# Performance work log

Measured on AMD Instinct MI355X. Metric: run time of the kernel, lower is better.

## Reference

```python
import jax, jax.numpy as jnp
import numpy as np

E, D, DFF = 8, 1024, 4096

def setup_inputs() -> dict:
    key = jax.random.key(0)
    ks = jax.random.split(key, 10)
    s = 0.02
    return {
        "x":  jax.random.normal(ks[0], (4, 2048, D), dtype=jnp.float32),
        "Wr": jax.random.normal(ks[1], (D, E), dtype=jnp.float32) * s,
        "br": jnp.zeros((E,), dtype=jnp.float32),
        "W1": jax.random.normal(ks[2], (E, D, DFF), dtype=jnp.float32) * s,
        "b1": jnp.zeros((E, DFF), dtype=jnp.float32),
        "W2": jax.random.normal(ks[3], (E, D, DFF), dtype=jnp.float32) * s,
        "b2": jnp.zeros((E, DFF), dtype=jnp.float32),
        "W3": jax.random.normal(ks[4], (E, DFF, D), dtype=jnp.float32) * s,
        "b3": jnp.zeros((E, D), dtype=jnp.float32),
    }

def reference(x, Wr, br, W1, b1, W2, b2, W3, b3):
    b, s, d = x.shape
    xt = x.reshape(b * s, d)                       # [T, D]
    logits = xt @ Wr + br                          # [T, E]
    pr, idx = jax.lax.top_k(logits, 2)             # [T, 2]
    w = jax.nn.softmax(pr, axis=-1)                # softmax over the 2 selected experts
    # combine weight per (token, expert): sum of routing weights where expert selected
    onehot = jax.nn.one_hot(idx, W1.shape[0], dtype=x.dtype)  # [T, 2, E]
    cw = jnp.einsum('tk,tke->te', w, onehot)       # [T, E]
    y = jnp.zeros_like(xt)
    for e in range(W1.shape[0]):                   # small fixed expert loop
        h = jax.nn.silu(xt @ W1[e] + b1[e]) * (xt @ W2[e] + b2[e])  # SwiGLU [T, DFF]
        y = y + (h @ W3[e] + b3[e]) * cw[:, e:e + 1]
    return y.reshape(b, s, d)
```

## Files before the change

### kernel.cpp

```cpp
#include <hip/hip_runtime.h>

#define T_TOK 8192
#define DIM   1024
#define DFF_  4096
#define NE    8
#define MAXT  144

typedef float  f32x4 __attribute__((ext_vector_type(4)));
typedef __bf16 b16x8 __attribute__((ext_vector_type(8)));

__device__ __forceinline__ unsigned short f2bf(float f) {
  union { float f; unsigned int u; } v; v.f = f;
  unsigned int r = v.u + 0x7fffu + ((v.u >> 16) & 1u);
  return (unsigned short)(r >> 16);
}

__device__ __forceinline__ void gload_lds16(const void* g, void* l) {
  __builtin_amdgcn_global_load_lds((const __attribute__((address_space(1))) void*)g,
                                   (__attribute__((address_space(3))) void*)l,
                                   16, 0, 0);
}

#define DRAIN_VMCNT() asm volatile("s_waitcnt vmcnt(0)" ::: "memory")

__global__ __launch_bounds__(256) void transpose_cvt(const float* __restrict__ src,
                                                     unsigned short* __restrict__ dst,
                                                     int R, int C) {
  __shared__ float tile[64][65];
  size_t mat = (size_t)blockIdx.z * R * C;
  int c0 = blockIdx.x * 64, r0 = blockIdx.y * 64;
  int lc = threadIdx.x & 63, q = threadIdx.x >> 6;
  const float* s = src + mat + (size_t)r0 * C + c0;
#pragma unroll
  for (int i = 0; i < 16; i++) {
    int r = q + i * 4;
    tile[r][lc] = s[(size_t)r * C + lc];
  }
  __syncthreads();
  unsigned short* d = dst + mat + (size_t)c0 * R + r0;
#pragma unroll
  for (int i = 0; i < 16; i++) {
    int cc = q + i * 4;
    d[(size_t)cc * R + lc] = f2bf(tile[lc][cc]);
  }
}

__global__ __launch_bounds__(256) void router_k(const float* __restrict__ x,
                                                const float* __restrict__ Wr,
                                                const float* __restrict__ br,
                                                unsigned short* __restrict__ Xbf,
                                                int* __restrict__ top2e,
                                                float* __restrict__ top2w) {
  int wid = threadIdx.x >> 6, lane = threadIdx.x & 63;
  int t = blockIdx.x * 4 + wid;
  const float* xr = x + (size_t)t * DIM;
  unsigned short* xb = Xbf + (size_t)t * DIM;
  float s[NE];
#pragma unroll
  for (int e = 0; e < NE; e++) s[e] = 0.f;
  for (int i = 0; i < DIM / 64; i++) {
    int dd = i * 64 + lane;
    float xv = xr[dd];
    xb[dd] = f2bf(xv);
    const float* w = Wr + (size_t)dd * NE;
#pragma unroll
    for (int e = 0; e < NE; e++) s[e] += xv * w[e];
  }
#pragma unroll
  for (int m = 32; m >= 1; m >>= 1) {
#pragma unroll
    for (int e = 0; e < NE; e++) s[e] += __shfl_xor(s[e], m, 64);
  }
  if (lane == 0) {
#pragma unroll
    for (int e = 0; e < NE; e++) s[e] += br[e];
    int e0 = 0;
#pragma unroll
    for (int e = 1; e < NE; e++) if (s[e] > s[e0]) e0 = e;
    int e1 = (e0 == 0) ? 1 : 0;
#pragma unroll
    for (int e = 0; e < NE; e++) if (e != e0 && s[e] > s[e1]) e1 = e;
    float w0 = 1.f / (1.f + expf(s[e1] - s[e0]));
    top2e[2 * t] = e0; top2e[2 * t + 1] = e1;
    top2w[2 * t] = w0; top2w[2 * t + 1] = 1.f - w0;
  }
}

__global__ __launch_bounds__(256) void count_k(const int* __restrict__ top2e,
                                               int* __restrict__ counts) {
  __shared__ int lcnt[NE];
  if (threadIdx.x < NE) lcnt[threadIdx.x] = 0;
  __syncthreads();
  int t = blockIdx.x * 256 + threadIdx.x;
  atomicAdd(&lcnt[top2e[2 * t]], 1);
  atomicAdd(&lcnt[top2e[2 * t + 1]], 1);
  __syncthreads();
  if (threadIdx.x < NE) atomicAdd(&counts[threadIdx.x], lcnt[threadIdx.x]);
}

__global__ void scan_build(int* __restrict__ ctrl) {
  if (threadIdx.x != 0 || blockIdx.x != 0) return;
  int* counts = ctrl;
  int* offsets = ctrl + 8;
  int* cursors = ctrl + 16;
  int* ntile = ctrl + 24;
  int* tileE = ctrl + 32;
  int* tileM = ctrl + 32 + MAXT;
  int o = 0;
  for (int e = 0; e < NE; e++) { offsets[e] = o; cursors[e] = o; o += counts[e]; }
  int nt = 0;
  for (int e = 0; e < NE; e++)
    for (int m0 = 0; m0 < counts[e]; m0 += 128) { tileE[nt] = e; tileM[nt] = m0; nt++; }
  ntile[0] = nt;
}

__global__ __launch_bounds__(256) void scatter_k(const int* __restrict__ top2e,
                                                 const float* __restrict__ top2w,
                                                 int* __restrict__ cursors,
                                                 int* __restrict__ list_tok,
                                                 float* __restrict__ list_w) {
  __shared__ int lcnt[NE];
  __shared__ int lbase[NE];
  int tid = threadIdx.x;
  if (tid < NE) lcnt[tid] = 0;
  __syncthreads();
  int t = blockIdx.x * 256 + tid;
  int e0 = top2e[2 * t], e1 = top2e[2 * t + 1];
  int r0 = atomicAdd(&lcnt[e0], 1);
  int r1 = atomicAdd(&lcnt[e1], 1);
  __syncthreads();
  if (tid < NE) lbase[tid] = atomicAdd(&cursors[tid], lcnt[tid]);
  __syncthreads();
  int p0 = lbase[e0] + r0, p1 = lbase[e1] + r1;
  list_tok[p0] = t; list_w[p0] = top2w[2 * t];
  list_tok[p1] = t; list_w[p1] = top2w[2 * t + 1];
}

__global__ __launch_bounds__(512) void gemm1_k(const unsigned short* __restrict__ Xbf,
                                               const unsigned short* __restrict__ W1T,
                                               const unsigned short* __restrict__ W2T,
                                               const float* __restrict__ b1,
                                               const float* __restrict__ b2,
                                               unsigned short* __restrict__ H,
                                               const int* __restrict__ list_tok,
                                               const int* __restrict__ ctrl) {
  const int* counts = ctrl; const int* offsets = ctrl + 8;
  const int* ntile = ctrl + 24;
  const int* tileE = ctrl + 32; const int* tileM = ctrl + 32 + MAXT;
  int bt = blockIdx.y;
  if (bt >= ntile[0]) return;
  int e = tileE[bt], m0 = tileM[bt];
  int Me = counts[e], off = offsets[e];
  int n0 = blockIdx.x * 128;

  __shared__ unsigned short lds[2][3 * 128 * 32];

  int tid = threadIdx.x, lane = tid & 63, wid = tid >> 6;
  int wr = wid >> 2, wc = wid & 3;

  const unsigned short* gsrc[3];
  unsigned ldsoff[3];
  {
    int lr = lane >> 2;
    int sc = ((lane & 3) ^ ((lane >> 3) & 3)) * 8;
#pragma unroll
    for (int j = 0; j < 3; j++) {
      int c = wid * 3 + j;
      ldsoff[j] = c * 512;
      if (c < 8) {
        int r = c * 16 + lr;
        int tok = (m0 + r < Me) ? list_tok[off + m0 + r] : list_tok[off];
        gsrc[j] = Xbf + (size_t)tok * DIM + sc;
      } else if (c < 16) {
        int n = n0 + (c - 8) * 16 + lr;
        gsrc[j] = W1T + ((size_t)e * DFF_ + n) * DIM + sc;
      } else {
        int n = n0 + (c - 16) * 16 + lr;
        gsrc[j] = W2T + ((size_t)e * DFF_ + n) * DIM + sc;
      }
    }
  }

  f32x4 acc1[4][2], acc2[4][2];
#pragma unroll
  for (int i = 0; i < 4; i++)
#pragma unroll
    for (int j = 0; j < 2; j++) {
      acc1[i][j] = f32x4{0.f, 0.f, 0.f, 0.f};
      acc2[i][j] = f32x4{0.f, 0.f, 0.f, 0.f};
    }

#pragma unroll
  for (int j = 0; j < 3; j++) gload_lds16(gsrc[j], (void*)(&lds[0][ldsoff[j]]));
  DRAIN_VMCNT();
  __syncthreads();

  int cur = 0;
  const int NK = DIM / 32;
  for (int kt = 0; kt < NK; kt++) {
    if (kt + 1 < NK) {
#pragma unroll
      for (int j = 0; j < 3; j++)
        gload_lds16(gsrc[j] + (kt + 1) * 32, (void*)(&lds[cur ^ 1][ldsoff[j]]));
    }
    const unsigned short* sA  = &lds[cur][0];
    const unsigned short* sB1 = sA + 4096;
    const unsigned short* sB2 = sA + 8192;
    int colg = lane >> 4;
    b16x8 aF[4], bF1[2], bF2[2];
#pragma unroll
    for (int fi = 0; fi < 4; fi++) {
      int row = wr * 64 + fi * 16 + (lane & 15);
      aF[fi] = *(const b16x8*)(sA + row * 32 + ((colg ^ ((row >> 1) & 3)) * 8));
    }
#pragma unroll
    for (int fj = 0; fj < 2; fj++) {
      int row = wc * 32 + fj * 16 + (lane & 15);
      int sw = (colg ^ ((row >> 1) & 3)) * 8;
      bF1[fj] = *(const b16x8*)(sB1 + row * 32 + sw);
      bF2[fj] = *(const b16x8*)(sB2 + row * 32 + sw);
    }
#pragma unroll
    for (int fi = 0; fi < 4; fi++)
#pragma unroll
      for (int fj = 0; fj < 2; fj++) {
        acc1[fi][fj] = __builtin_amdgcn_mfma_f32_16x16x32_bf16(aF[fi], bF1[fj], acc1[fi][fj], 0, 0, 0);
        acc2[fi][fj] = __builtin_amdgcn_mfma_f32_16x16x32_bf16(aF[fi], bF2[fj], acc2[fi][fj], 0, 0, 0);
      }
    DRAIN_VMCNT();
    __syncthreads();
    cur ^= 1;
  }

#pragma unroll
  for (int fi = 0; fi < 4; fi++)
#pragma unroll
    for (int fj = 0; fj < 2; fj++) {
      int col = n0 + wc * 32 + fj * 16 + (lane & 15);
      float bb1 = b1[e * DFF_ + col], bb2 = b2[e * DFF_ + col];
      int rbase = wr * 64 + fi * 16 + (lane >> 4) * 4;
#pragma unroll
      for (int r = 0; r < 4; r++) {
        int rr = rbase + r;
        if (m0 + rr < Me) {
          float c1 = acc1[fi][fj][r] + bb1;
          float c2 = acc2[fi][fj][r] + bb2;
          float h = c1 * c2 / (1.f + __expf(-c1));
          H[(size_t)(off + m0 + rr) * DFF_ + col] = f2bf(h);
        }
      }
    }
}

__global__ __launch_bounds__(512) void gemm2_k(const unsigned short* __restrict__ H,
                                               const unsigned short* __restrict__ W3T,
                                               const float* __restrict__ b3,
                                               const int* __restrict__ list_tok,
                                               const float* __restrict__ list_w,
                                               float* __restrict__ y,
                                               const int* __restrict__ ctrl) {
  const int* counts = ctrl; const int* offsets = ctrl + 8;
  const int* ntile = ctrl + 24;
  const int* tileE = ctrl + 32; const int* tileM = ctrl + 32 + MAXT;
  int bt = blockIdx.y;
  if (bt >= ntile[0]) return;
  int e = tileE[bt], m0 = tileM[bt];
  int Me = counts[e], off = offsets[e];
  int n0 = blockIdx.x * 128;

  __shared__ unsigned short lds[2][2 * 128 * 64];

  int tid = threadIdx.x, lane = tid & 63, wid = tid >> 6;
  int wr = wid >> 2, wc = wid & 3;

  const unsigned short* gsrc[4];
  unsigned ldsoff[4];
  {
    int lr = lane >> 3;
    int sc = ((lane & 7) ^ (lane >> 3)) * 8;
#pragma unroll
    for (int j = 0; j < 4; j++) {
      int c = wid * 4 + j;
      ldsoff[j] = c * 512;
      if (c < 16) {
        int r = c * 8 + lr;
        int pos = (m0 + r < Me) ? (off + m0 + r) : off;
        gsrc[j] = H + (size_t)pos * DFF_ + sc;
      } else {
        int n = n0 + (c - 16) * 8 + lr;
        gsrc[j] = W3T + ((size_t)e * DIM + n) * DFF_ + sc;
      }
    }
  }

  f32x4 acc[4][2];
#pragma unroll
  for (int i = 0; i < 4; i++)
#pragma unroll
    for (int j = 0; j < 2; j++) acc[i][j] = f32x4{0.f, 0.f, 0.f, 0.f};

#pragma unroll
  for (int j = 0; j < 4; j++) gload_lds16(gsrc[j], (void*)(&lds[0][ldsoff[j]]));
  DRAIN_VMCNT();
  __syncthreads();

  int cur = 0;
  const int NK = DFF_ / 64;
  for (int kt = 0; kt < NK; kt++) {
    if (kt + 1 < NK) {
#pragma unroll
      for (int j = 0; j < 4; j++)
        gload_lds16(gsrc[j] + (kt + 1) * 64, (void*)(&lds[cur ^ 1][ldsoff[j]]));
    }
    const unsigned short* sA = &lds[cur][0];
    const unsigned short* sB = sA + 128 * 64;
    int colg = lane >> 4;
#pragma unroll
    for (int kk = 0; kk < 2; kk++) {
      b16x8 aF[4], bF[2];
#pragma unroll
      for (int fi = 0; fi < 4; fi++) {
        int row = wr * 64 + fi * 16 + (lane & 15);
        aF[fi] = *(const b16x8*)(sA + row * 64 + (((kk * 4 + colg) ^ (row & 7)) * 8));
      }
#pragma unroll
      for (int fj = 0; fj < 2; fj++) {
        int row = wc * 32 + fj * 16 + (lane & 15);
        bF[fj] = *(const b16x8*)(sB + row * 64 + (((kk * 4 + colg) ^ (row & 7)) * 8));
      }
#pragma unroll
      for (int fi = 0; fi < 4; fi++)
#pragma unroll
        for (int fj = 0; fj < 2; fj++)
          acc[fi][fj] = __builtin_amdgcn_mfma_f32_16x16x32_bf16(aF[fi], bF[fj], acc[fi][fj], 0, 0, 0);
    }
    DRAIN_VMCNT();
    __syncthreads();
    cur ^= 1;
  }

#pragma unroll
  for (int fi = 0; fi < 4; fi++)
#pragma unroll
    for (int fj = 0; fj < 2; fj++) {
      int col = n0 + wc * 32 + fj * 16 + (lane & 15);
      float bb3 = b3[e * DIM + col];
      int rbase = wr * 64 + fi * 16 + (lane >> 4) * 4;
#pragma unroll
      for (int r = 0; r < 4; r++) {
        int rr = rbase + r;
        if (m0 + rr < Me) {
          int pos = off + m0 + rr;
          float v = list_w[pos] * (acc[fi][fj][r] + bb3);
          atomicAdd(&y[(size_t)list_tok[pos] * DIM + col], v);
        }
      }
    }
}

extern "C" void kernel_launch(void* const* d_in, const int* in_sizes, int n_in,
                              void* d_out, int out_size, void* d_ws, size_t ws_size,
                              hipStream_t stream) {
  (void)in_sizes; (void)n_in; (void)ws_size;
  const float* x  = (const float*)d_in[0];
  const float* Wr = (const float*)d_in[1];
  const float* br = (const float*)d_in[2];
  const float* W1 = (const float*)d_in[3];
  const float* b1 = (const float*)d_in[4];
  const float* W2 = (const float*)d_in[5];
  const float* b2 = (const float*)d_in[6];
  const float* W3 = (const float*)d_in[7];
  const float* b3 = (const float*)d_in[8];
  float* y = (float*)d_out;
  char* ws = (char*)d_ws;

  const size_t matB = (size_t)NE * DFF_ * DIM * 2;
  size_t oW1T = 0;
  size_t oW2T = oW1T + matB;
  size_t oXbf = oW2T + matB;
  size_t oH   = oXbf + (size_t)T_TOK * DIM * 2;
  size_t oT2e = oH + (size_t)2 * T_TOK * DFF_ * 2;
  size_t oT2w = oT2e + (size_t)2 * T_TOK * 4;
  size_t oLtk = oT2w + (size_t)2 * T_TOK * 4;
  size_t oLw  = oLtk + (size_t)2 * T_TOK * 4;
  size_t oCtl = oLw + (size_t)2 * T_TOK * 4;

  unsigned short* W1T = (unsigned short*)(ws + oW1T);
  unsigned short* W2T = (unsigned short*)(ws + oW2T);
  unsigned short* W3T = (unsigned short*)(ws + oW1T);
  unsigned short* Xbf = (unsigned short*)(ws + oXbf);
  unsigned short* Hb  = (unsigned short*)(ws + oH);
  int*   top2e = (int*)(ws + oT2e);
  float* top2w = (float*)(ws + oT2w);
  int*   ltok  = (int*)(ws + oLtk);
  float* lw    = (float*)(ws + oLw);
  int*   ctrl  = (int*)(ws + oCtl);

  hipMemsetAsync(y, 0, (size_t)out_size * 4, stream);
  hipMemsetAsync(ctrl, 0, (32 + 2 * MAXT) * 4, stream);

  transpose_cvt<<<dim3(DFF_ / 64, DIM / 64, NE), 256, 0, stream>>>(W1, W1T, DIM, DFF_);
  transpose_cvt<<<dim3(DFF_ / 64, DIM / 64, NE), 256, 0, stream>>>(W2, W2T, DIM, DFF_);
  router_k<<<dim3(T_TOK / 4), 256, 0, stream>>>(x, Wr, br, Xbf, top2e, top2w);
  count_k<<<dim3(T_TOK / 256), 256, 0, stream>>>(top2e, ctrl);
  scan_build<<<dim3(1), 64, 0, stream>>>(ctrl);
  scatter_k<<<dim3(T_TOK / 256), 256, 0, stream>>>(top2e, top2w, ctrl + 16, ltok, lw);
  gemm1_k<<<dim3(DFF_ / 128, MAXT - 8), 512, 0, stream>>>(Xbf, W1T, W2T, b1, b2, Hb, ltok, ctrl);
  transpose_cvt<<<dim3(DIM / 64, DFF_ / 64, NE), 256, 0, stream>>>(W3, W3T, DFF_, DIM);
  gemm2_k<<<dim3(DIM / 128, MAXT - 8), 512, 0, stream>>>(Hb, W3T, b3, ltok, lw, y, ctrl);
}
```

Measured before the change: 764.6 us.

## Triple-buffer LDS pipelines in both expert GEMMs with partial vmcnt waits

Result: slower. 806.6 us (+5.5%).

```diff
diff --git a/kernel.cpp b/kernel.cpp
--- a/kernel.cpp
+++ b/kernel.cpp
@@ -21,7 +21,7 @@
                                    16, 0, 0);
 }
 
-#define DRAIN_VMCNT() asm volatile("s_waitcnt vmcnt(0)" ::: "memory")
+#define WAITCNT(n) asm volatile("s_waitcnt vmcnt(" #n ")" ::: "memory")
 
 __global__ __launch_bounds__(256) void transpose_cvt(const float* __restrict__ src,
                                                      unsigned short* __restrict__ dst,
@@ -153,7 +153,7 @@
   int Me = counts[e], off = offsets[e];
   int n0 = blockIdx.x * 128;
 
-  __shared__ unsigned short lds[2][3 * 128 * 32];
+  __shared__ unsigned short lds[3][3 * 128 * 32];
 
   int tid = threadIdx.x, lane = tid & 63, wid = tid >> 6;
   int wr = wid >> 2, wc = wid & 3;
@@ -190,22 +190,10 @@
       acc2[i][j] = f32x4{0.f, 0.f, 0.f, 0.f};
     }
 
-#pragma unroll
-  for (int j = 0; j < 3; j++) gload_lds16(gsrc[j], (void*)(&lds[0][ldsoff[j]]));
-  DRAIN_VMCNT();
-  __syncthreads();
-
-  int cur = 0;
-  const int NK = DIM / 32;
-  for (int kt = 0; kt < NK; kt++) {
-    if (kt + 1 < NK) {
-#pragma unroll
-      for (int j = 0; j < 3; j++)
-        gload_lds16(gsrc[j] + (kt + 1) * 32, (void*)(&lds[cur ^ 1][ldsoff[j]]));
-    }
-    const unsigned short* sA  = &lds[cur][0];
-    const unsigned short* sB1 = sA + 4096;
-    const unsigned short* sB2 = sA + 8192;
+  auto compute = [&](const unsigned short* base) {
+    const unsigned short* sA  = base;
+    const unsigned short* sB1 = base + 4096;
+    const unsigned short* sB2 = base + 8192;
     int colg = lane >> 4;
     b16x8 aF[4], bF1[2], bF2[2];
 #pragma unroll
@@ -220,6 +208,7 @@
       bF1[fj] = *(const b16x8*)(sB1 + row * 32 + sw);
       bF2[fj] = *(const b16x8*)(sB2 + row * 32 + sw);
     }
+    __builtin_amdgcn_s_setprio(1);
 #pragma unroll
     for (int fi = 0; fi < 4; fi++)
 #pragma unroll
@@ -227,10 +216,35 @@
         acc1[fi][fj] = __builtin_amdgcn_mfma_f32_16x16x32_bf16(aF[fi], bF1[fj], acc1[fi][fj], 0, 0, 0);
         acc2[fi][fj] = __builtin_amdgcn_mfma_f32_16x16x32_bf16(aF[fi], bF2[fj], acc2[fi][fj], 0, 0, 0);
       }
-    DRAIN_VMCNT();
+    __builtin_amdgcn_s_setprio(0);
+  };
+
+  const int NK = DIM / 32;
+#pragma unroll
+  for (int j = 0; j < 3; j++) gload_lds16(gsrc[j], (void*)(&lds[0][ldsoff[j]]));
+#pragma unroll
+  for (int j = 0; j < 3; j++) gload_lds16(gsrc[j] + 32, (void*)(&lds[1][ldsoff[j]]));
+
+  int cbuf = 0, pbuf = 2;
+  for (int kt = 0; kt < NK - 2; kt++) {
+#pragma unroll
+    for (int j = 0; j < 3; j++)
+      gload_lds16(gsrc[j] + (kt + 2) * 32, (void*)(&lds[pbuf][ldsoff[j]]));
+    WAITCNT(6);
     __syncthreads();
-    cur ^= 1;
-  }
+    compute(&lds[cbuf][0]);
+    __syncthreads();
+    cbuf = (cbuf == 2) ? 0 : cbuf + 1;
+    pbuf = (pbuf == 2) ? 0 : pbuf + 1;
+  }
+  WAITCNT(3);
+  __syncthreads();
+  compute(&lds[cbuf][0]);
+  __syncthreads();
+  cbuf = (cbuf == 2) ? 0 : cbuf + 1;
+  WAITCNT(0);
+  __syncthreads();
+  compute(&lds[cbuf][0]);
 
 #pragma unroll
   for (int fi = 0; fi < 4; fi++)
@@ -268,26 +282,26 @@
   int Me = counts[e], off = offsets[e];
   int n0 = blockIdx.x * 128;
 
-  __shared__ unsigned short lds[2][2 * 128 * 64];
+  __shared__ unsigned short lds[3][2 * 128 * 32];
 
   int tid = threadIdx.x, lane = tid & 63, wid = tid >> 6;
   int wr = wid >> 2, wc = wid & 3;
 
-  const unsigned short* gsrc[4];
-  unsigned ldsoff[4];
+  const unsigned short* gsrc[2];
+  unsigned ldsoff[2];
   {
-    int lr = lane >> 3;
-    int sc = ((lane & 7) ^ (lane >> 3)) * 8;
-#pragma unroll
-    for (int j = 0; j < 4; j++) {
-      int c = wid * 4 + j;
+    int lr = lane >> 2;
+    int sc = ((lane & 3) ^ ((lane >> 3) & 3)) * 8;
+#pragma unroll
+    for (int j = 0; j < 2; j++) {
+      int c = wid * 2 + j;
       ldsoff[j] = c * 512;
-      if (c < 16) {
-        int r = c * 8 + lr;
+      if (c < 8) {
+        int r = c * 16 + lr;
         int pos = (m0 + r < Me) ? (off + m0 + r) : off;
         gsrc[j] = H + (size_t)pos * DFF_ + sc;
       } else {
-        int n = n0 + (c - 16) * 8 + lr;
+        int n = n0 + (c - 8) * 16 + lr;
         gsrc[j] = W3T + ((size_t)e * DIM + n) * DFF_ + sc;
       }
     }
@@ -299,45 +313,56 @@
 #pragma unroll
     for (int j = 0; j < 2; j++) acc[i][j] = f32x4{0.f, 0.f, 0.f, 0.f};
 
-#pragma unroll
-  for (int j = 0; j < 4; j++) gload_lds16(gsrc[j], (void*)(&lds[0][ldsoff[j]]));
-  DRAIN_VMCNT();
-  __syncthreads();
-
-  int cur = 0;
-  const int NK = DFF_ / 64;
-  for (int kt = 0; kt < NK; kt++) {
-    if (kt + 1 < NK) {
-#pragma unroll
-      for (int j = 0; j < 4; j++)
-        gload_lds16(gsrc[j] + (kt + 1) * 64, (void*)(&lds[cur ^ 1][ldsoff[j]]));
-    }
-    const unsigned short* sA = &lds[cur][0];
-    const unsigned short* sB = sA + 128 * 64;
+  auto compute = [&](const unsigned short* base) {
+    const unsigned short* sA = base;
+    const unsigned short* sB = base + 4096;
     int colg = lane >> 4;
-#pragma unroll
-    for (int kk = 0; kk < 2; kk++) {
-      b16x8 aF[4], bF[2];
-#pragma unroll
-      for (int fi = 0; fi < 4; fi++) {
-        int row = wr * 64 + fi * 16 + (lane & 15);
-        aF[fi] = *(const b16x8*)(sA + row * 64 + (((kk * 4 + colg) ^ (row & 7)) * 8));
-      }
-#pragma unroll
-      for (int fj = 0; fj < 2; fj++) {
-        int row = wc * 32 + fj * 16 + (lane & 15);
-        bF[fj] = *(const b16x8*)(sB + row * 64 + (((kk * 4 + colg) ^ (row & 7)) * 8));
-      }
-#pragma unroll
-      for (int fi = 0; fi < 4; fi++)
-#pragma unroll
-        for (int fj = 0; fj < 2; fj++)
-          acc[fi][fj] = __builtin_amdgcn_mfma_f32_16x16x32_bf16(aF[fi], bF[fj], acc[fi][fj], 0, 0, 0);
-    }
-    DRAIN_VMCNT();
+    b16x8 aF[4], bF[2];
+#pragma unroll
+    for (int fi = 0; fi < 4; fi++) {
+      int row = wr * 64 + fi * 16 + (lane & 15);
+      aF[fi] = *(const b16x8*)(sA + row * 32 + ((colg ^ ((row >> 1) & 3)) * 8));
+    }
+#pragma unroll
+    for (int fj = 0; fj < 2; fj++) {
+      int row = wc * 32 + fj * 16 + (lane & 15);
+      bF[fj] = *(const b16x8*)(sB + row * 32 + ((colg ^ ((row >> 1) & 3)) * 8));
+    }
+    __builtin_amdgcn_s_setprio(1);
+#pragma unroll
+    for (int fi = 0; fi < 4; fi++)
+#pragma unroll
+      for (int fj = 0; fj < 2; fj++)
+        acc[fi][fj] = __builtin_amdgcn_mfma_f32_16x16x32_bf16(aF[fi], bF[fj], acc[fi][fj], 0, 0, 0);
+    __builtin_amdgcn_s_setprio(0);
+  };
+
+  const int NK = DFF_ / 32;
+#pragma unroll
+  for (int j = 0; j < 2; j++) gload_lds16(gsrc[j], (void*)(&lds[0][ldsoff[j]]));
+#pragma unroll
+  for (int j = 0; j < 2; j++) gload_lds16(gsrc[j] + 32, (void*)(&lds[1][ldsoff[j]]));
+
+  int cbuf = 0, pbuf = 2;
+  for (int kt = 0; kt < NK - 2; kt++) {
+#pragma unroll
+    for (int j = 0; j < 2; j++)
+      gload_lds16(gsrc[j] + (kt + 2) * 32, (void*)(&lds[pbuf][ldsoff[j]]));
+    WAITCNT(4);
     __syncthreads();
-    cur ^= 1;
-  }
+    compute(&lds[cbuf][0]);
+    __syncthreads();
+    cbuf = (cbuf == 2) ? 0 : cbuf + 1;
+    pbuf = (pbuf == 2) ? 0 : pbuf + 1;
+  }
+  WAITCNT(2);
+  __syncthreads();
+  compute(&lds[cbuf][0]);
+  __syncthreads();
+  cbuf = (cbuf == 2) ? 0 : cbuf + 1;
+  WAITCNT(0);
+  __syncthreads();
+  compute(&lds[cbuf][0]);
 
 #pragma unroll
   for (int fi = 0; fi < 4; fi++)
```

## Widen GEMM N-tiles to 256 and precompute LDS fragment offsets

Applied to the files above, without the earlier changes.

Measured after the change: 906.4 us. 1.19x slower.

```diff
diff --git a/kernel.cpp b/kernel.cpp
--- a/kernel.cpp
+++ b/kernel.cpp
@@ -151,47 +151,83 @@
   if (bt >= ntile[0]) return;
   int e = tileE[bt], m0 = tileM[bt];
   int Me = counts[e], off = offsets[e];
-  int n0 = blockIdx.x * 128;
-
-  __shared__ unsigned short lds[2][3 * 128 * 32];
+  int n0 = blockIdx.x * 256;
+
+  __shared__ unsigned short lds[2][20480];
 
   int tid = threadIdx.x, lane = tid & 63, wid = tid >> 6;
   int wr = wid >> 2, wc = wid & 3;
 
-  const unsigned short* gsrc[3];
-  unsigned ldsoff[3];
+  const unsigned short* gsrc[5];
+  unsigned ldsoff[5];
   {
     int lr = lane >> 2;
     int sc = ((lane & 3) ^ ((lane >> 3) & 3)) * 8;
 #pragma unroll
-    for (int j = 0; j < 3; j++) {
-      int c = wid * 3 + j;
+    for (int j = 0; j < 5; j++) {
+      int c = wid * 5 + j;
       ldsoff[j] = c * 512;
       if (c < 8) {
         int r = c * 16 + lr;
         int tok = (m0 + r < Me) ? list_tok[off + m0 + r] : list_tok[off];
         gsrc[j] = Xbf + (size_t)tok * DIM + sc;
-      } else if (c < 16) {
+      } else if (c < 24) {
         int n = n0 + (c - 8) * 16 + lr;
         gsrc[j] = W1T + ((size_t)e * DFF_ + n) * DIM + sc;
       } else {
-        int n = n0 + (c - 16) * 16 + lr;
+        int n = n0 + (c - 24) * 16 + lr;
         gsrc[j] = W2T + ((size_t)e * DFF_ + n) * DIM + sc;
       }
     }
   }
 
-  f32x4 acc1[4][2], acc2[4][2];
+  unsigned aoff[4], boff[4];
+  {
+    int colg = lane >> 4;
+#pragma unroll
+    for (int fi = 0; fi < 4; fi++) {
+      int row = wr * 64 + fi * 16 + (lane & 15);
+      aoff[fi] = row * 32 + ((colg ^ ((row >> 1) & 3)) * 8);
+    }
+#pragma unroll
+    for (int fj = 0; fj < 4; fj++) {
+      int row = wc * 64 + fj * 16 + (lane & 15);
+      boff[fj] = row * 32 + ((colg ^ ((row >> 1) & 3)) * 8);
+    }
+  }
+
+  f32x4 acc1[4][4], acc2[4][4];
 #pragma unroll
   for (int i = 0; i < 4; i++)
 #pragma unroll
-    for (int j = 0; j < 2; j++) {
+    for (int j = 0; j < 4; j++) {
       acc1[i][j] = f32x4{0.f, 0.f, 0.f, 0.f};
       acc2[i][j] = f32x4{0.f, 0.f, 0.f, 0.f};
     }
 
-#pragma unroll
-  for (int j = 0; j < 3; j++) gload_lds16(gsrc[j], (void*)(&lds[0][ldsoff[j]]));
+  auto compute = [&](const unsigned short* base) {
+    const unsigned short* sA  = base;
+    const unsigned short* sB1 = base + 4096;
+    const unsigned short* sB2 = base + 12288;
+    b16x8 aF[4], bF1[4], bF2[4];
+#pragma unroll
+    for (int fi = 0; fi < 4; fi++) aF[fi] = *(const b16x8*)(sA + aoff[fi]);
+#pragma unroll
+    for (int fj = 0; fj < 4; fj++) {
+      bF1[fj] = *(const b16x8*)(sB1 + boff[fj]);
+      bF2[fj] = *(const b16x8*)(sB2 + boff[fj]);
+    }
+#pragma unroll
+    for (int fi = 0; fi < 4; fi++)
+#pragma unroll
+      for (int fj = 0; fj < 4; fj++) {
+        acc1[fi][fj] = __builtin_amdgcn_mfma_f32_16x16x32_bf16(aF[fi], bF1[fj], acc1[fi][fj], 0, 0, 0);
+        acc2[fi][fj] = __builtin_amdgcn_mfma_f32_16x16x32_bf16(aF[fi], bF2[fj], acc2[fi][fj], 0, 0, 0);
+      }
+  };
+
+#pragma unroll
+  for (int j = 0; j < 5; j++) gload_lds16(gsrc[j], (void*)(&lds[0][ldsoff[j]]));
   DRAIN_VMCNT();
   __syncthreads();
 
@@ -200,33 +236,10 @@
   for (int kt = 0; kt < NK; kt++) {
     if (kt + 1 < NK) {
 #pragma unroll
-      for (int j = 0; j < 3; j++)
+      for (int j = 0; j < 5; j++)
         gload_lds16(gsrc[j] + (kt + 1) * 32, (void*)(&lds[cur ^ 1][ldsoff[j]]));
     }
-    const unsigned short* sA  = &lds[cur][0];
-    const unsigned short* sB1 = sA + 4096;
-    const unsigned short* sB2 = sA + 8192;
-    int colg = lane >> 4;
-    b16x8 aF[4], bF1[2], bF2[2];
-#pragma unroll
-    for (int fi = 0; fi < 4; fi++) {
-      int row = wr * 64 + fi * 16 + (lane & 15);
-      aF[fi] = *(const b16x8*)(sA + row * 32 + ((colg ^ ((row >> 1) & 3)) * 8));
-    }
-#pragma unroll
-    for (int fj = 0; fj < 2; fj++) {
-      int row = wc * 32 + fj * 16 + (lane & 15);
-      int sw = (colg ^ ((row >> 1) & 3)) * 8;
-      bF1[fj] = *(const b16x8*)(sB1 + row * 32 + sw);
-      bF2[fj] = *(const b16x8*)(sB2 + row * 32 + sw);
-    }
-#pragma unroll
-    for (int fi = 0; fi < 4; fi++)
-#pragma unroll
-      for (int fj = 0; fj < 2; fj++) {
-        acc1[fi][fj] = __builtin_amdgcn_mfma_f32_16x16x32_bf16(aF[fi], bF1[fj], acc1[fi][fj], 0, 0, 0);
-        acc2[fi][fj] = __builtin_amdgcn_mfma_f32_16x16x32_bf16(aF[fi], bF2[fj], acc2[fi][fj], 0, 0, 0);
-      }
+    compute(&lds[cur][0]);
     DRAIN_VMCNT();
     __syncthreads();
     cur ^= 1;
@@ -235,8 +248,8 @@
 #pragma unroll
   for (int fi = 0; fi < 4; fi++)
 #pragma unroll
-    for (int fj = 0; fj < 2; fj++) {
-      int col = n0 + wc * 32 + fj * 16 + (lane & 15);
+    for (int fj = 0; fj < 4; fj++) {
+      int col = n0 + wc * 64 + fj * 16 + (lane & 15);
       float bb1 = b1[e * DFF_ + col], bb2 = b2[e * DFF_ + col];
       int rbase = wr * 64 + fi * 16 + (lane >> 4) * 4;
 #pragma unroll
@@ -266,74 +279,83 @@
   if (bt >= ntile[0]) return;
   int e = tileE[bt], m0 = tileM[bt];
   int Me = counts[e], off = offsets[e];
-  int n0 = blockIdx.x * 128;
-
-  __shared__ unsigned short lds[2][2 * 128 * 64];
+  int n0 = blockIdx.x * 256;
+
+  __shared__ unsigned short lds[2][12288];
 
   int tid = threadIdx.x, lane = tid & 63, wid = tid >> 6;
   int wr = wid >> 2, wc = wid & 3;
 
-  const unsigned short* gsrc[4];
-  unsigned ldsoff[4];
+  const unsigned short* gsrc[3];
+  unsigned ldsoff[3];
   {
-    int lr = lane >> 3;
-    int sc = ((lane & 7) ^ (lane >> 3)) * 8;
-#pragma unroll
-    for (int j = 0; j < 4; j++) {
-      int c = wid * 4 + j;
+    int lr = lane >> 2;
+    int sc = ((lane & 3) ^ ((lane >> 3) & 3)) * 8;
+#pragma unroll
+    for (int j = 0; j < 3; j++) {
+      int c = wid * 3 + j;
       ldsoff[j] = c * 512;
-      if (c < 16) {
-        int r = c * 8 + lr;
+      if (c < 8) {
+        int r = c * 16 + lr;
         int pos = (m0 + r < Me) ? (off + m0 + r) : off;
         gsrc[j] = H + (size_t)pos * DFF_ + sc;
       } else {
-        int n = n0 + (c - 16) * 8 + lr;
+        int n = n0 + (c - 8) * 16 + lr;
         gsrc[j] = W3T + ((size_t)e * DIM + n) * DFF_ + sc;
       }
     }
   }
 
-  f32x4 acc[4][2];
+  unsigned aoff[4], boff[4];
+  {
+    int colg = lane >> 4;
+#pragma unroll
+    for (int fi = 0; fi < 4; fi++) {
+      int row = wr * 64 + fi * 16 + (lane & 15);
+      aoff[fi] = row * 32 + ((colg ^ ((row >> 1) & 3)) * 8);
+    }
+#pragma unroll
+    for (int fj = 0; fj < 4; fj++) {
+      int row = wc * 64 + fj * 16 + (lane & 15);
+      boff[fj] = row * 32 + ((colg ^ ((row >> 1) & 3)) * 8);
+    }
+  }
+
+  f32x4 acc[4][4];
 #pragma unroll
   for (int i = 0; i < 4; i++)
 #pragma unroll
-    for (int j = 0; j < 2; j++) acc[i][j] = f32x4{0.f, 0.f, 0.f, 0.f};
-
-#pragma unroll
-  for (int j = 0; j < 4; j++) gload_lds16(gsrc[j], (void*)(&lds[0][ldsoff[j]]));
+    for (int j = 0; j < 4; j++) acc[i][j] = f32x4{0.f, 0.f, 0.f, 0.f};
+
+  auto compute = [&](const unsigned short* base) {
+    const unsigned short* sA = base;
+    const unsigned short* sB = base + 4096;
+    b16x8 aF[4], bF[4];
+#pragma unroll
+    for (int fi = 0; fi < 4; fi++) aF[fi] = *(const b16x8*)(sA + aoff[fi]);
+#pragma unroll
+    for (int fj = 0; fj < 4; fj++) bF[fj] = *(const b16x8*)(sB + boff[fj]);
+#pragma unroll
+    for (int fi = 0; fi < 4; fi++)
+#pragma unroll
+      for (int fj = 0; fj < 4; fj++)
+        acc[fi][fj] = __builtin_amdgcn_mfma_f32_16x16x32_bf16(aF[fi], bF[fj], acc[fi][fj], 0, 0, 0);
+  };
+
+#pragma unroll
+  for (int j = 0; j < 3; j++) gload_lds16(gsrc[j], (void*)(&lds[0][ldsoff[j]]));
   DRAIN_VMCNT();
   __syncthreads();
 
   int cur = 0;
-  const int NK = DFF_ / 64;
+  const int NK = DFF_ / 32;
   for (int kt = 0; kt < NK; kt++) {
     if (kt + 1 < NK) {
 #pragma unroll
-      for (int j = 0; j < 4; j++)
-        gload_lds16(gsrc[j] + (kt + 1) * 64, (void*)(&lds[cur ^ 1][ldsoff[j]]));
-    }
-    const unsigned short* sA = &lds[cur][0];
-    const unsigned short* sB = sA + 128 * 64;
-    int colg = lane >> 4;
-#pragma unroll
-    for (int kk = 0; kk < 2; kk++) {
-      b16x8 aF[4], bF[2];
-#pragma unroll
-      for (int fi = 0; fi < 4; fi++) {
-        int row = wr * 64 + fi * 16 + (lane & 15);
-        aF[fi] = *(const b16x8*)(sA + row * 64 + (((kk * 4 + colg) ^ (row & 7)) * 8));
-      }
-#pragma unroll
-      for (int fj = 0; fj < 2; fj++) {
-        int row = wc * 32 + fj * 16 + (lane & 15);
-        bF[fj] = *(const b16x8*)(sB + row * 64 + (((kk * 4 + colg) ^ (row & 7)) * 8));
-      }
-#pragma unroll
-      for (int fi = 0; fi < 4; fi++)
-#pragma unroll
-        for (int fj = 0; fj < 2; fj++)
-          acc[fi][fj] = __builtin_amdgcn_mfma_f32_16x16x32_bf16(aF[fi], bF[fj], acc[fi][fj], 0, 0, 0);
-    }
+      for (int j = 0; j < 3; j++)
+        gload_lds16(gsrc[j] + (kt + 1) * 32, (void*)(&lds[cur ^ 1][ldsoff[j]]));
+    }
+    compute(&lds[cur][0]);
     DRAIN_VMCNT();
     __syncthreads();
     cur ^= 1;
@@ -342,8 +364,8 @@
 #pragma unroll
   for (int fi = 0; fi < 4; fi++)
 #pragma unroll
-    for (int fj = 0; fj < 2; fj++) {
-      int col = n0 + wc * 32 + fj * 16 + (lane & 15);
+    for (int fj = 0; fj < 4; fj++) {
+      int col = n0 + wc * 64 + fj * 16 + (lane & 15);
       float bb3 = b3[e * DIM + col];
       int rbase = wr * 64 + fi * 16 + (lane >> 4) * 4;
 #pragma unroll
@@ -405,7 +427,7 @@
   count_k<<<dim3(T_TOK / 256), 256, 0, stream>>>(top2e, ctrl);
   scan_build<<<dim3(1), 64, 0, stream>>>(ctrl);
   scatter_k<<<dim3(T_TOK / 256), 256, 0, stream>>>(top2e, top2w, ctrl + 16, ltok, lw);
-  gemm1_k<<<dim3(DFF_ / 128, MAXT - 8), 512, 0, stream>>>(Xbf, W1T, W2T, b1, b2, Hb, ltok, ctrl);
+  gemm1_k<<<dim3(DFF_ / 256, MAXT - 8), 512, 0, stream>>>(Xbf, W1T, W2T, b1, b2, Hb, ltok, ctrl);
   transpose_cvt<<<dim3(DIM / 64, DFF_ / 64, NE), 256, 0, stream>>>(W3, W3T, DFF_, DIM);
-  gemm2_k<<<dim3(DIM / 128, MAXT - 8), 512, 0, stream>>>(Hb, W3T, b3, ltok, lw, y, ctrl);
-}
+  gemm2_k<<<dim3(DIM / 256, MAXT - 8), 512, 0, stream>>>(Hb, W3T, b3, ltok, lw, y, ctrl);
+}
```
